# Optimization experiments

Hardware: AMD Instinct MI355X
Metric: run time of the kernel (lower is better)

The kernel has to match this reference:

```python
import jax, jax.numpy as jnp
import numpy as np

M_DIM = 1024
H_DIM = 1024
NEG = -1e9


def setup_inputs() -> dict:
    key = jax.random.key(0)
    ks = jax.random.split(key, 9)
    B, S = 4, 2048
    q = jax.random.normal(ks[0], (B, S, M_DIM), dtype=jnp.float32)
    k = jax.random.normal(ks[1], (B, S, M_DIM), dtype=jnp.float32)
    v = jax.random.normal(ks[2], (B, S, M_DIM), dtype=jnp.float32)
    attention_mask = jnp.ones((B, S), dtype=jnp.int32)
    sc = 1.0 / np.sqrt(M_DIM)
    Wq_w = jax.random.normal(ks[3], (H_DIM, M_DIM), dtype=jnp.float32) * sc
    Wq_b = jnp.zeros((H_DIM,), dtype=jnp.float32)
    Wk_w = jax.random.normal(ks[4], (H_DIM, M_DIM), dtype=jnp.float32) * sc
    Wk_b = jnp.zeros((H_DIM,), dtype=jnp.float32)
    Wv_w = jax.random.normal(ks[5], (H_DIM, M_DIM), dtype=jnp.float32) * sc
    Wv_b = jnp.zeros((H_DIM,), dtype=jnp.float32)
    return {"q": q, "k": k, "v": v, "attention_mask": attention_mask,
            "Wq_w": Wq_w, "Wq_b": Wq_b, "Wk_w": Wk_w, "Wk_b": Wk_b,
            "Wv_w": Wv_w, "Wv_b": Wv_b}


def reference(q, k, v, attention_mask, Wq_w, Wq_b, Wk_w, Wk_b, Wv_w, Wv_b):
    # Linear projections (torch Linear: x @ W.T + b)
    qh = jnp.einsum('bsm,hm->bsh', q, Wq_w) + Wq_b
    kh = jnp.einsum('bsm,hm->bsh', k, Wk_w) + Wk_b
    vh = jnp.einsum('bsm,hm->bsh', v, Wv_w) + Wv_b
    # Scaled dot-product scores: [B, Sq, Sk]
    scores = jnp.einsum('bqh,bkh->bqk', qh, kh) / jnp.sqrt(jnp.float32(H_DIM))
    # Padding mask: attention_mask [B, Sk] -> [B, 1, Sk]
    pad = attention_mask.astype(bool)[:, None, :]
    scores = jnp.where(pad, scores, NEG)
    # Causal mask (apply_mask=True)
    Sq, Sk = scores.shape[1], scores.shape[2]
    causal = jnp.tril(jnp.ones((Sq, Sk), dtype=bool))
    scores = jnp.where(causal[None, :, :], scores, NEG)
    attn = jax.nn.softmax(scores, axis=-1)
    out = jnp.einsum('bqk,bkh->bqh', attn, vh)
    # dropout is identity in eval mode
    return out
```

## Files before the change

### kernel.cpp

```cpp
#include <hip/hip_runtime.h>
#include <stdint.h>


typedef __attribute__((ext_vector_type(8))) short s8v;
typedef __attribute__((ext_vector_type(4))) float f4v;

__device__ __forceinline__ unsigned short f2bf(float f) {
    union { float f; unsigned u; } v; v.f = f;
    unsigned u = v.u;
    u = u + 0x7fffu + ((u >> 16) & 1u);
    return (unsigned short)(u >> 16);
}

__device__ __forceinline__ void gld_lds16(const void* gptr, void* lptr) {
    __builtin_amdgcn_global_load_lds(
        (const __attribute__((address_space(1))) unsigned int*)(uintptr_t)gptr,
        (__attribute__((address_space(3))) unsigned int*)(unsigned int)(uintptr_t)lptr,
        16, 0, 0);
}

__global__ __launch_bounds__(256) void convert_all(
    const float* __restrict__ q, const float* __restrict__ k, const float* __restrict__ v,
    const float* __restrict__ wq, const float* __restrict__ wk, const float* __restrict__ wv,
    unsigned short* __restrict__ qb, unsigned short* __restrict__ kb, unsigned short* __restrict__ vb,
    unsigned short* __restrict__ wqb, unsigned short* __restrict__ wkb, unsigned short* __restrict__ wvb,
    float* __restrict__ l)
{
    int b = blockIdx.x;
    if (b >= 27648) {
        int li = (b - 27648) * 256 + threadIdx.x;
        l[li] = 0.f;
        return;
    }
    const float* src; unsigned short* dst; int blk;
    if (b < 8192)       { src = q;  dst = qb;  blk = b; }
    else if (b < 16384) { src = k;  dst = kb;  blk = b - 8192; }
    else if (b < 24576) { src = v;  dst = vb;  blk = b - 16384; }
    else if (b < 25600) { src = wq; dst = wqb; blk = b - 24576; }
    else if (b < 26624) { src = wk; dst = wkb; blk = b - 25600; }
    else                { src = wv; dst = wvb; blk = b - 26624; }
    size_t idx = (size_t)blk * 1024 + (size_t)threadIdx.x * 4;
    float4 f = *(const float4*)(src + idx);
    ushort4 o = make_ushort4(f2bf(f.x), f2bf(f.y), f2bf(f.z), f2bf(f.w));
    *(ushort4*)(dst + idx) = o;
}

__device__ __forceinline__ void gemm_tiles(
    const unsigned short* __restrict__ A, int lda,
    const unsigned short* __restrict__ Bt, int ldb,
    int m0, int n0, int kTiles,
    unsigned short* As, unsigned short* Bs,
    f4v acc[4][4])
{
    const int t    = threadIdx.x;
    const int lane = t & 63;
    const int wave = t >> 6;
    const int wm   = (wave >> 1) * 64;
    const int wn   = (wave & 1) * 64;
    const int l15  = lane & 15;
    const int quad = lane >> 4;

    const int c0 = t, c1 = t + 256;
    unsigned short* As0 = As + (c0 & ~63) * 8;
    unsigned short* As1 = As + (c1 & ~63) * 8;
    unsigned short* Bs0 = Bs + (c0 & ~63) * 8;
    unsigned short* Bs1 = Bs + (c1 & ~63) * 8;
    const unsigned short* Ag0 = A  + (size_t)(m0 + (c0 >> 2)) * lda + (c0 & 3) * 8;
    const unsigned short* Ag1 = A  + (size_t)(m0 + (c1 >> 2)) * lda + (c1 & 3) * 8;
    const unsigned short* Bg0 = Bt + (size_t)(n0 + (c0 >> 2)) * ldb + (c0 & 3) * 8;
    const unsigned short* Bg1 = Bt + (size_t)(n0 + (c1 >> 2)) * ldb + (c1 & 3) * 8;

    const unsigned short* a_base = As + quad * 8;
    const unsigned short* b_base = Bs + quad * 8;

    for (int kt = 0; kt < kTiles; ++kt) {
        gld_lds16(Ag0, As0);
        gld_lds16(Ag1, As1);
        gld_lds16(Bg0, Bs0);
        gld_lds16(Bg1, Bs1);
        Ag0 += 32; Ag1 += 32; Bg0 += 32; Bg1 += 32;
        __syncthreads();
        s8v af[4], bf[4];
        #pragma unroll
        for (int i = 0; i < 4; ++i)
            af[i] = *(const s8v*)(a_base + (wm + i * 16 + l15) * 32);
        #pragma unroll
        for (int j = 0; j < 4; ++j)
            bf[j] = *(const s8v*)(b_base + (wn + j * 16 + l15) * 32);
        #pragma unroll
        for (int i = 0; i < 4; ++i)
            #pragma unroll
            for (int j = 0; j < 4; ++j)
                acc[i][j] = __builtin_amdgcn_mfma_f32_16x16x32_bf16(af[i], bf[j], acc[i][j], 0, 0, 0);
        __syncthreads();
    }
}

#define ACC_INIT  f4v acc[4][4]; { f4v z = {0.f,0.f,0.f,0.f}; \
    _Pragma("unroll") for (int i = 0; i < 4; ++i) \
    _Pragma("unroll") for (int j = 0; j < 4; ++j) acc[i][j] = z; }

#define LANE_VARS \
    const int lane = threadIdx.x & 63; const int wave = threadIdx.x >> 6; \
    const int wm = (wave >> 1) * 64;  const int wn = (wave & 1) * 64; \
    const int l15 = lane & 15;        const int quad = lane >> 4;

__global__ __launch_bounds__(256) void proj_kernel(
    const unsigned short* __restrict__ qb, const unsigned short* __restrict__ wqb,
    const float* __restrict__ bq, unsigned short* __restrict__ QH,
    const unsigned short* __restrict__ kb, const unsigned short* __restrict__ wkb,
    const float* __restrict__ bk, unsigned short* __restrict__ KH,
    const unsigned short* __restrict__ vb, const unsigned short* __restrict__ wvb,
    const float* __restrict__ bv, unsigned short* __restrict__ VHT)
{
    const int z = blockIdx.z;
    const unsigned short* X; const unsigned short* W; const float* bias; unsigned short* Y;
    if (z == 0)      { X = qb; W = wqb; bias = bq; Y = QH; }
    else if (z == 1) { X = kb; W = wkb; bias = bk; Y = KH; }
    else             { X = vb; W = wvb; bias = bv; Y = VHT; }

    __shared__ __align__(16) unsigned short As[128 * 32];
    __shared__ __align__(16) unsigned short Bs[128 * 32];
    const int m0 = blockIdx.x * 128;
    const int n0 = blockIdx.y * 128;
    ACC_INIT;
    gemm_tiles(X, 1024, W, 1024, m0, n0, 32, As, Bs, acc);
    LANE_VARS;
    #pragma unroll
    for (int i = 0; i < 4; ++i) {
        int row = m0 + wm + i * 16 + quad * 4;
        #pragma unroll
        for (int j = 0; j < 4; ++j) {
            int col = n0 + wn + j * 16 + l15;
            float bvv = bias[col];
            if (z != 2) {
                #pragma unroll
                for (int r = 0; r < 4; ++r)
                    Y[(size_t)(row + r) * 1024 + col] = f2bf(acc[i][j][r] + bvv);
            } else {
                int bb = row >> 11;
                int s  = row & 2047;
                ushort4 o = make_ushort4(f2bf(acc[i][j][0] + bvv), f2bf(acc[i][j][1] + bvv),
                                         f2bf(acc[i][j][2] + bvv), f2bf(acc[i][j][3] + bvv));
                *(ushort4*)(Y + (size_t)bb * (1024 * 2048) + (size_t)col * 2048 + s) = o;
            }
        }
    }
}

__global__ __launch_bounds__(256) void score_kernel(
    const unsigned short* __restrict__ QH, const unsigned short* __restrict__ KH,
    const int* __restrict__ mask, unsigned short* __restrict__ P, float* __restrict__ lsum)
{
    const int kt = blockIdx.x, qt = blockIdx.y, b = blockIdx.z;
    if (kt > qt) return;
    __shared__ __align__(16) unsigned short As[128 * 32];
    __shared__ __align__(16) unsigned short Bs[128 * 32];
    const unsigned short* A  = QH + (size_t)b * 2048 * 1024;
    const unsigned short* Bt = KH + (size_t)b * 2048 * 1024;
    unsigned short* Pb = P + (size_t)b * 2048 * 2048;
    float* lb = lsum + b * 2048;
    const int* mb = mask + b * 2048;
    const int m0 = qt * 128, n0 = kt * 128;
    ACC_INIT;
    gemm_tiles(A, 1024, Bt, 1024, m0, n0, 32, As, Bs, acc);
    LANE_VARS;
    float rs[4][4];
    #pragma unroll
    for (int i = 0; i < 4; ++i)
        #pragma unroll
        for (int r = 0; r < 4; ++r) rs[i][r] = 0.f;
    #pragma unroll
    for (int i = 0; i < 4; ++i) {
        int qbase = m0 + wm + i * 16 + quad * 4;
        #pragma unroll
        for (int j = 0; j < 4; ++j) {
            int kg = n0 + wn + j * 16 + l15;
            int mv = mb[kg];
            #pragma unroll
            for (int r = 0; r < 4; ++r) {
                float s = acc[i][j][r] * 0.03125f;
                float p = (mv && (kg <= qbase + r)) ? __expf(s) : 0.f;
                Pb[(size_t)(qbase + r) * 2048 + kg] = f2bf(p);
                rs[i][r] += p;
            }
        }
    }
    #pragma unroll
    for (int i = 0; i < 4; ++i)
        #pragma unroll
        for (int r = 0; r < 4; ++r) {
            float v_ = rs[i][r];
            v_ += __shfl_xor(v_, 1);
            v_ += __shfl_xor(v_, 2);
            v_ += __shfl_xor(v_, 4);
            v_ += __shfl_xor(v_, 8);
            if (l15 == 0)
                atomicAdd(&lb[m0 + wm + i * 16 + quad * 4 + r], v_);
        }
}

__constant__ int pv_qt[24] = {15,15, 7,14,14,13,13, 6,12,12,11,11, 5,10,10, 9, 9, 4, 8, 8, 3, 2, 1, 0};
__constant__ int pv_ks[24] = { 0,32, 0, 0,30, 0,28, 0, 0,26, 0,24, 0, 0,22, 0,20, 0, 0,18, 0, 0, 0, 0};
__constant__ int pv_kc[24] = {32,32,32,30,30,28,28,28,26,26,24,24,24,22,22,20,20,20,18,18,16,12, 8, 4};

__global__ __launch_bounds__(256) void pv_kernel(
    const unsigned short* __restrict__ P, const unsigned short* __restrict__ VHT,
    const float* __restrict__ lsum, float* __restrict__ Out, float* __restrict__ Part)
{
    const int nt = blockIdx.x, y = blockIdx.y, b = blockIdx.z;
    const int qt = pv_qt[y], kstart = pv_ks[y], kcount = pv_kc[y];

    __shared__ __align__(16) unsigned short As[128 * 32];
    __shared__ __align__(16) unsigned short Bs[128 * 32];
    const unsigned short* A  = P   + (size_t)b * 2048 * 2048 + (size_t)kstart * 32;
    const unsigned short* Bt = VHT + (size_t)b * 1024 * 2048 + (size_t)kstart * 32;
    const float* lb = lsum + b * 2048;
    const int m0 = qt * 128, n0 = nt * 128;
    ACC_INIT;
    gemm_tiles(A, 2048, Bt, 2048, m0, n0, kcount, As, Bs, acc);
    LANE_VARS;
    float* dst; int rowoff;
    if (kstart == 0) { dst = Out  + (size_t)b * 2048 * 1024; rowoff = 0; }
    else             { dst = Part + (size_t)b * 1024 * 1024; rowoff = -1024; }
    #pragma unroll
    for (int i = 0; i < 4; ++i) {
        int q0 = m0 + wm + i * 16 + quad * 4;
        float inv[4];
        #pragma unroll
        for (int r = 0; r < 4; ++r) inv[r] = 1.0f / lb[q0 + r];
        #pragma unroll
        for (int j = 0; j < 4; ++j) {
            int h = n0 + wn + j * 16 + l15;
            #pragma unroll
            for (int r = 0; r < 4; ++r)
                dst[(size_t)(q0 + r + rowoff) * 1024 + h] = acc[i][j][r] * inv[r];
        }
    }
}

__global__ __launch_bounds__(256) void add_partial(
    float4* __restrict__ Out4, const float4* __restrict__ Part4)
{
    int i = blockIdx.x * 256 + threadIdx.x;
    int b = i >> 18;
    int rem = i & 262143;
    int oi = b * 524288 + 262144 + rem;
    float4 o = Out4[oi], p = Part4[i];
    o.x += p.x; o.y += p.y; o.z += p.z; o.w += p.w;
    Out4[oi] = o;
}

extern "C" void kernel_launch(void* const* d_in, const int* in_sizes, int n_in,
                              void* d_out, int out_size, void* d_ws, size_t ws_size,
                              hipStream_t stream)
{
    const float* q    = (const float*)d_in[0];
    const float* k    = (const float*)d_in[1];
    const float* v    = (const float*)d_in[2];
    const int*   mask = (const int*)d_in[3];
    const float* Wq   = (const float*)d_in[4];
    const float* bq   = (const float*)d_in[5];
    const float* Wk   = (const float*)d_in[6];
    const float* bk   = (const float*)d_in[7];
    const float* Wv   = (const float*)d_in[8];
    const float* bv   = (const float*)d_in[9];
    float* out = (float*)d_out;

    char* ws = (char*)d_ws;
    size_t off = 0;
    auto take = [&](size_t bytes) { char* p = ws + off; off += (bytes + 255) & ~(size_t)255; return p; };
    unsigned short* qb  = (unsigned short*)take(8192ull * 1024 * 2);
    unsigned short* kb  = (unsigned short*)take(8192ull * 1024 * 2);
    unsigned short* vb  = (unsigned short*)take(8192ull * 1024 * 2);
    unsigned short* wqb = (unsigned short*)take(1024ull * 1024 * 2);
    unsigned short* wkb = (unsigned short*)take(1024ull * 1024 * 2);
    unsigned short* wvb = (unsigned short*)take(1024ull * 1024 * 2);
    unsigned short* QH  = (unsigned short*)take(8192ull * 1024 * 2);
    unsigned short* KH  = (unsigned short*)take(8192ull * 1024 * 2);
    unsigned short* VHT = (unsigned short*)take(8192ull * 1024 * 2);
    unsigned short* P   = (unsigned short*)take(4ull * 2048 * 2048 * 2);
    float*          l   = (float*)take(4ull * 2048 * 4);
    float*          Part = (float*)qb;

    convert_all<<<27680, 256, 0, stream>>>(q, k, v, Wq, Wk, Wv,
                                           qb, kb, vb, wqb, wkb, wvb, l);
    proj_kernel<<<dim3(64, 8, 3), 256, 0, stream>>>(qb, wqb, bq, QH,
                                                    kb, wkb, bk, KH,
                                                    vb, wvb, bv, VHT);
    score_kernel<<<dim3(16, 16, 4), 256, 0, stream>>>(QH, KH, mask, P, l);
    pv_kernel<<<dim3(8, 24, 4), 256, 0, stream>>>(P, VHT, l, out, Part);
    add_partial<<<4096, 256, 0, stream>>>((float4*)out, (const float4*)Part);
}
```

Baseline: 338.9 us.

## Double-buffer LDS tiles in GEMM loop and compact causal score grid

The shared GEMM tile loop now uses two LDS buffers. The next k-tile's global-to-LDS loads are issued before computing on the current tile, leaving one barrier per iteration instead of two. This aims to overlap memory latency with MFMA work, at the cost of doubling LDS use per block, which may lower occupancy. The score kernel also launches only the lower-triangular tiles (136 per batch) instead of a full 16x16 grid with early exits, removing idle blocks.

```diff
diff --git a/kernel.cpp b/kernel.cpp
--- a/kernel.cpp
+++ b/kernel.cpp
@@ -73,26 +73,34 @@
     const unsigned short* a_base = As + quad * 8;
     const unsigned short* b_base = Bs + quad * 8;
 
+    gld_lds16(Ag0, As0);
+    gld_lds16(Ag1, As1);
+    gld_lds16(Bg0, Bs0);
+    gld_lds16(Bg1, Bs1);
+
     for (int kt = 0; kt < kTiles; ++kt) {
-        gld_lds16(Ag0, As0);
-        gld_lds16(Ag1, As1);
-        gld_lds16(Bg0, Bs0);
-        gld_lds16(Bg1, Bs1);
+        __syncthreads();
         Ag0 += 32; Ag1 += 32; Bg0 += 32; Bg1 += 32;
-        __syncthreads();
+        if (kt + 1 < kTiles) {
+            const int nb = ((kt + 1) & 1) * 4096;
+            gld_lds16(Ag0, As0 + nb);
+            gld_lds16(Ag1, As1 + nb);
+            gld_lds16(Bg0, Bs0 + nb);
+            gld_lds16(Bg1, Bs1 + nb);
+        }
+        const int cb = (kt & 1) * 4096;
         s8v af[4], bf[4];
         #pragma unroll
         for (int i = 0; i < 4; ++i)
-            af[i] = *(const s8v*)(a_base + (wm + i * 16 + l15) * 32);
+            af[i] = *(const s8v*)(a_base + cb + (wm + i * 16 + l15) * 32);
         #pragma unroll
         for (int j = 0; j < 4; ++j)
-            bf[j] = *(const s8v*)(b_base + (wn + j * 16 + l15) * 32);
+            bf[j] = *(const s8v*)(b_base + cb + (wn + j * 16 + l15) * 32);
         #pragma unroll
         for (int i = 0; i < 4; ++i)
             #pragma unroll
             for (int j = 0; j < 4; ++j)
                 acc[i][j] = __builtin_amdgcn_mfma_f32_16x16x32_bf16(af[i], bf[j], acc[i][j], 0, 0, 0);
-        __syncthreads();
     }
 }
 
@@ -119,8 +127,8 @@
     else if (z == 1) { X = kb; W = wkb; bias = bk; Y = KH; }
     else             { X = vb; W = wvb; bias = bv; Y = VHT; }
 
-    __shared__ __align__(16) unsigned short As[128 * 32];
-    __shared__ __align__(16) unsigned short Bs[128 * 32];
+    __shared__ __align__(16) unsigned short As[2 * 128 * 32];
+    __shared__ __align__(16) unsigned short Bs[2 * 128 * 32];
     const int m0 = blockIdx.x * 128;
     const int n0 = blockIdx.y * 128;
     ACC_INIT;
@@ -152,10 +160,14 @@
     const unsigned short* __restrict__ QH, const unsigned short* __restrict__ KH,
     const int* __restrict__ mask, unsigned short* __restrict__ P, float* __restrict__ lsum)
 {
-    const int kt = blockIdx.x, qt = blockIdx.y, b = blockIdx.z;
-    if (kt > qt) return;
-    __shared__ __align__(16) unsigned short As[128 * 32];
-    __shared__ __align__(16) unsigned short Bs[128 * 32];
+    const int b = blockIdx.y;
+    int tq = blockIdx.x;
+    int qt = 0;
+    while ((qt + 1) * (qt + 2) / 2 <= tq) ++qt;
+    const int kt = tq - qt * (qt + 1) / 2;
+
+    __shared__ __align__(16) unsigned short As[2 * 128 * 32];
+    __shared__ __align__(16) unsigned short Bs[2 * 128 * 32];
     const unsigned short* A  = QH + (size_t)b * 2048 * 1024;
     const unsigned short* Bt = KH + (size_t)b * 2048 * 1024;
     unsigned short* Pb = P + (size_t)b * 2048 * 2048;
@@ -211,8 +223,8 @@
     const int nt = blockIdx.x, y = blockIdx.y, b = blockIdx.z;
     const int qt = pv_qt[y], kstart = pv_ks[y], kcount = pv_kc[y];
 
-    __shared__ __align__(16) unsigned short As[128 * 32];
-    __shared__ __align__(16) unsigned short Bs[128 * 32];
+    __shared__ __align__(16) unsigned short As[2 * 128 * 32];
+    __shared__ __align__(16) unsigned short Bs[2 * 128 * 32];
     const unsigned short* A  = P   + (size_t)b * 2048 * 2048 + (size_t)kstart * 32;
     const unsigned short* Bt = VHT + (size_t)b * 1024 * 2048 + (size_t)kstart * 32;
     const float* lb = lsum + b * 2048;
@@ -288,7 +300,7 @@
     proj_kernel<<<dim3(64, 8, 3), 256, 0, stream>>>(qb, wqb, bq, QH,
                                                     kb, wkb, bk, KH,
                                                     vb, wvb, bv, VHT);
-    score_kernel<<<dim3(16, 16, 4), 256, 0, stream>>>(QH, KH, mask, P, l);
+    score_kernel<<<dim3(136, 4), 256, 0, stream>>>(QH, KH, mask, P, l);
     pv_kernel<<<dim3(8, 24, 4), 256, 0, stream>>>(P, VHT, l, out, Part);
     add_partial<<<4096, 256, 0, stream>>>((float4*)out, (const float4*)Part);
 }
```

Measured after the change: 316.2 us. 1.07x faster.
